# Optimization experiments

Hardware: AMD Instinct MI355X
Metric: run time of the kernel (lower is better)

The kernel has to match this reference:

```python
import jax, jax.numpy as jnp
import numpy as np

N_NODES = 100000
MAX_CHILD = 8
X_SIZE = 128
H_SIZE = 128
N_TYPES = 8
W_SCALE = 0.05  # keep gates out of saturation


def setup_inputs() -> dict:
    key = jax.random.key(0)
    ks = jax.random.split(key, 8)
    return {
        "x": jax.random.normal(ks[0], (N_NODES, X_SIZE), jnp.float32),
        "n_h": jax.random.normal(ks[1], (N_NODES, MAX_CHILD, H_SIZE), jnp.float32),
        "n_c": jax.random.normal(ks[2], (N_NODES, MAX_CHILD, H_SIZE), jnp.float32),
        "type_id": jax.random.randint(ks[3], (N_NODES,), 0, N_TYPES, jnp.int64),
        "W_iou": jax.random.normal(ks[4], (N_TYPES, X_SIZE, 3 * H_SIZE), jnp.float32) * W_SCALE,
        "U_iou": jax.random.normal(ks[5], (N_TYPES, H_SIZE, 3 * H_SIZE), jnp.float32) * W_SCALE,
        "b_iou": jnp.zeros((N_TYPES, 3 * H_SIZE), jnp.float32),
        "U_f": jax.random.normal(ks[6], (N_TYPES, H_SIZE, H_SIZE), jnp.float32) * W_SCALE,
        "b_f": jnp.zeros((N_TYPES, H_SIZE), jnp.float32),
    }


def reference(x, n_h, n_c, type_id, W_iou, U_iou, b_iou, U_f, b_f):
    # x: [N, X], n_h/n_c: [N, K, H] child mailbox, type_id: [N]
    N, K, H = n_h.shape
    T = W_iou.shape[0]
    h_sum = n_h.sum(axis=1)  # child-sum is linear -> aggregate before GEMM [N, H]

    # --- reduce_func: masked per-type child aggregation ---
    iou_aggr = jnp.zeros((N, 3 * H), x.dtype)
    c_aggr = jnp.zeros((N, H), x.dtype)
    for t in range(T):
        m = (type_id == t)[:, None]
        iou_t = h_sum @ U_iou[t]                                   # [N, 3H]
        f = jax.nn.sigmoid(jnp.einsum("nkh,hg->nkg", n_h, U_f[t]) + b_f[t])
        c_t = (f * n_c).sum(axis=1)                                # [N, H]
        iou_aggr = jnp.where(m, iou_t, iou_aggr)
        c_aggr = jnp.where(m, c_t, c_aggr)

    # --- apply_node_func: masked per-type node states ---
    h_out = jnp.zeros((N, H), x.dtype)
    c_out = jnp.zeros((N, H), x.dtype)
    for t in range(T):
        m = (type_id == t)[:, None]
        iou = x @ W_iou[t] + iou_aggr + b_iou[t]                   # [N, 3H]
        i_g, o_g, u_g = jnp.split(iou, 3, axis=1)
        c_t = jax.nn.sigmoid(i_g) * jnp.tanh(u_g) + c_aggr
        h_t = jax.nn.sigmoid(o_g) * jnp.tanh(c_t)
        h_out = jnp.where(m, h_t, h_out)
        c_out = jnp.where(m, c_t, c_out)
    return h_out, c_out
```

## Files before the change

kernel.cpp:

```cpp
#include <hip/hip_runtime.h>
#include <hip/hip_bf16.h>
#include <stdint.h>

typedef __bf16 bf16x8 __attribute__((ext_vector_type(8)));
typedef float  f32x4  __attribute__((ext_vector_type(4)));

#define H    128
#define KCH  8
#define NT   8
#define BM   32

#define WS_TILET  2048
#define WS_IDX    16384
#define WS_UF     458752
#define WS_W      720896

__device__ __forceinline__ float fsigm(float v){ return 1.f/(1.f+__expf(-v)); }
__device__ __forceinline__ float ftanh(float v){
  v = fminf(fmaxf(v,-15.f),15.f);
  float e = __expf(2.f*v);
  return (e-1.f)/(e+1.f);
}

__global__ void k_init(int* ws){ if (threadIdx.x < 40) ws[threadIdx.x] = 0; }

__global__ void k_detect(const int* __restrict__ type_id, int* ws){
  __shared__ int nz;
  if (threadIdx.x == 0) nz = 0;
  __syncthreads();
  int v = type_id[threadIdx.x];
  if ((threadIdx.x & 1) && v != 0) atomicAdd(&nz, 1);
  __syncthreads();
  if (threadIdx.x == 0) ws[25] = (nz == 0) ? 2 : 1;
}

__global__ void k_count(const int* __restrict__ type_id, int* __restrict__ ws, int N){
  __shared__ int h[NT];
  int tid = threadIdx.x;
  if (tid < NT) h[tid] = 0;
  __syncthreads();
  int stride = ws[25];
  int i = blockIdx.x*blockDim.x + tid;
  if (i < N) atomicAdd(&h[type_id[(size_t)i*stride]], 1);
  __syncthreads();
  if (tid < NT) atomicAdd(&ws[tid], h[tid]);
}

__global__ void k_scan(int* m){
  int s = 0;
  for (int t=0;t<NT;++t){
    m[16+t] = s;
    m[8+t]  = s;
    m[26+t] = s + m[t];
    s += ((m[t]+BM-1)/BM)*BM;
  }
  m[24] = s;
}

__global__ void k_scatter(const int* __restrict__ type_id, int* __restrict__ ws, int N){
  __shared__ int h[NT], base[NT];
  int tid = threadIdx.x;
  if (tid < NT) h[tid] = 0;
  __syncthreads();
  int stride = ws[25];
  int i = blockIdx.x*blockDim.x + tid;
  int t = 0, lp = 0;
  if (i < N){ t = type_id[(size_t)i*stride]; lp = atomicAdd(&h[t], 1); }
  __syncthreads();
  if (tid < NT) base[tid] = atomicAdd(&ws[8+tid], h[tid]);
  __syncthreads();
  if (i < N) ws[(WS_IDX/4) + base[t] + lp] = i;
}

__global__ void k_tiletype(int* ws, int ntiles){
  int i = blockIdx.x*256 + threadIdx.x;
  if (i >= ntiles) return;
  const int* op = ws + 16;
  int p = i*BM, t = -1;
  if (p < op[8]){
    for (int s=0;s<NT;++s) if (p >= op[s] && p < op[s+1]) t = s;
  }
  ws[(WS_TILET/4) + i] = t;
}

__global__ void k_prep_uf(const float* __restrict__ U_f, char* __restrict__ ws){
  int gid = blockIdx.x*256 + threadIdx.x;
  if (gid >= NT*128*16) return;
  int sp = gid & 15, c = (gid>>4) & 127, t = gid >> 11;
  int kbase = 8*(sp ^ (c & 7));
  const float* src = U_f + ((size_t)t*H + kbase)*H + c;
  bf16x8 v;
  #pragma unroll
  for (int j=0;j<8;++j) v[j] = (__bf16)src[(size_t)j*H];
  *(bf16x8*)(ws + WS_UF + (size_t)gid*16) = v;
}

__global__ void k_prep_w(const float* __restrict__ W_iou, const float* __restrict__ U_iou,
                         char* __restrict__ ws){
  int gid = blockIdx.x*256 + threadIdx.x;
  if (gid >= NT*384*32) return;
  int sp = gid & 31, col = (gid>>5) % 384, t = gid / (384*32);
  int K0 = sp*8;
  bf16x8 v;
  #pragma unroll
  for (int j=0;j<8;++j){
    int K = K0 + j;
    float f = (K < H) ? W_iou[((size_t)t*H + K)*(3*H) + col]
                      : U_iou[((size_t)t*H + (K-H))*(3*H) + col];
    v[j] = (__bf16)f;
  }
  *(bf16x8*)(ws + WS_W + (size_t)gid*16) = v;
}

__global__ __launch_bounds__(256,3) void k_fused(
  const float* __restrict__ x, const float* __restrict__ n_h, const float* __restrict__ n_c,
  const float* __restrict__ b_iou, const float* __restrict__ b_f,
  const char* __restrict__ ws, float* __restrict__ out, int N)
{
  __shared__ __align__(16) char lds[49152];
  const int* meta = (const int*)ws;
  int tile = blockIdx.x;
  int t = ((const int*)(ws + WS_TILET))[tile];
  if (t < 0) return;
  int ev = meta[26 + t];
  const int* idx = (const int*)(ws + WS_IDX);

  int tid = threadIdx.x;
  int lane = tid & 63, wave = tid >> 6;
  int rw = wave & 1, cw = wave >> 1;
  int l15 = lane & 15, l4 = lane >> 4;
  int base = tile*BM;

  int mrow = tid >> 3, mcol = (tid & 7) * 16;
  int mpos = base + mrow;
  int mnode = (mpos < ev) ? idx[mpos] : 0;

  int npos = base + rw*16 + l15;
  bool valn = npos < ev;
  int nd = valn ? idx[npos] : 0;
  const float* ncb = n_c + (size_t)nd*(KCH*H);
  int ocb[4]; f32x4 bf4[4];
  #pragma unroll
  for (int st=0; st<4; ++st){
    ocb[st] = cw*64 + st*16 + 4*l4;
    bf4[st] = *(const f32x4*)(b_f + t*H + ocb[st]);
  }

  {
    const char* src = ws + WS_UF + (size_t)t*32768;
    #pragma unroll
    for (int it=0; it<8; ++it){
      bf16x8 v = *(const bf16x8*)(src + it*4096 + tid*16);
      *(bf16x8*)(lds + it*4096 + tid*16) = v;
    }
  }

  const float* nh_base = n_h + (size_t)mnode*(KCH*H) + mcol;

  float hsum[16];
  #pragma unroll
  for (int j=0;j<16;++j) hsum[j] = 0.f;
  f32x4 cacc[4];
  #pragma unroll
  for (int st=0;st<4;++st) cacc[st] = (f32x4){0.f,0.f,0.f,0.f};

  int arow = rw*16 + l15;
  int aswz = (arow & 7) << 4;
  int mswz = (mrow & 7) << 4;

  {
    const float4* p = (const float4*)nh_base;
    float4 a0=p[0], a1=p[1], a2=p[2], a3=p[3];
    hsum[0]+=a0.x;  hsum[1]+=a0.y;  hsum[2]+=a0.z;  hsum[3]+=a0.w;
    hsum[4]+=a1.x;  hsum[5]+=a1.y;  hsum[6]+=a1.z;  hsum[7]+=a1.w;
    hsum[8]+=a2.x;  hsum[9]+=a2.y;  hsum[10]+=a2.z; hsum[11]+=a2.w;
    hsum[12]+=a3.x; hsum[13]+=a3.y; hsum[14]+=a3.z; hsum[15]+=a3.w;
    bf16x8 w0, w1;
    w0[0]=(__bf16)a0.x; w0[1]=(__bf16)a0.y; w0[2]=(__bf16)a0.z; w0[3]=(__bf16)a0.w;
    w0[4]=(__bf16)a1.x; w0[5]=(__bf16)a1.y; w0[6]=(__bf16)a1.z; w0[7]=(__bf16)a1.w;
    w1[0]=(__bf16)a2.x; w1[1]=(__bf16)a2.y; w1[2]=(__bf16)a2.z; w1[3]=(__bf16)a2.w;
    w1[4]=(__bf16)a3.x; w1[5]=(__bf16)a3.y; w1[6]=(__bf16)a3.z; w1[7]=(__bf16)a3.w;
    *(bf16x8*)(lds + 32768 + mrow*256 + (( mcol*2      ) ^ mswz)) = w0;
    *(bf16x8*)(lds + 32768 + mrow*256 + (( mcol*2 + 16 ) ^ mswz)) = w1;
  }
  __syncthreads();

  #pragma unroll 1
  for (int k=0;k<KCH;++k){
    const int cur = 32768 + (k&1)*8192;
    const int nxt = 32768 + ((k+1)&1)*8192;

    f32x4 nc4[4];
    #pragma unroll
    for (int st=0;st<4;++st) nc4[st] = *(const f32x4*)(ncb + (size_t)k*H + ocb[st]);

    float4 b0,b1,b2,b3;
    if (k < KCH-1){
      const float4* p = (const float4*)(nh_base + (size_t)(k+1)*H);
      b0=p[0]; b1=p[1]; b2=p[2]; b3=p[3];
    }

    f32x4 fa[4];
    #pragma unroll
    for (int st=0;st<4;++st) fa[st] = (f32x4){0.f,0.f,0.f,0.f};
    __builtin_amdgcn_s_setprio(1);
    #pragma unroll
    for (int kk=0; kk<4; ++kk){
      int kb = kk*64 + l4*16;
      bf16x8 bnh = *(const bf16x8*)(lds + cur + arow*256 + (kb ^ aswz));
      #pragma unroll
      for (int st=0;st<4;++st){
        int c = cw*64 + st*16 + l15;
        bf16x8 auf = *(const bf16x8*)(lds + c*256 + (kb ^ ((c&7)<<4)));
        fa[st] = __builtin_amdgcn_mfma_f32_16x16x32_bf16(auf, bnh, fa[st], 0,0,0);
      }
    }
    __builtin_amdgcn_s_setprio(0);

    if (k < KCH-1){
      hsum[0]+=b0.x;  hsum[1]+=b0.y;  hsum[2]+=b0.z;  hsum[3]+=b0.w;
      hsum[4]+=b1.x;  hsum[5]+=b1.y;  hsum[6]+=b1.z;  hsum[7]+=b1.w;
      hsum[8]+=b2.x;  hsum[9]+=b2.y;  hsum[10]+=b2.z; hsum[11]+=b2.w;
      hsum[12]+=b3.x; hsum[13]+=b3.y; hsum[14]+=b3.z; hsum[15]+=b3.w;
      bf16x8 w0, w1;
      w0[0]=(__bf16)b0.x; w0[1]=(__bf16)b0.y; w0[2]=(__bf16)b0.z; w0[3]=(__bf16)b0.w;
      w0[4]=(__bf16)b1.x; w0[5]=(__bf16)b1.y; w0[6]=(__bf16)b1.z; w0[7]=(__bf16)b1.w;
      w1[0]=(__bf16)b2.x; w1[1]=(__bf16)b2.y; w1[2]=(__bf16)b2.z; w1[3]=(__bf16)b2.w;
      w1[4]=(__bf16)b3.x; w1[5]=(__bf16)b3.y; w1[6]=(__bf16)b3.z; w1[7]=(__bf16)b3.w;
      *(bf16x8*)(lds + nxt + mrow*256 + (( mcol*2      ) ^ mswz)) = w0;
      *(bf16x8*)(lds + nxt + mrow*256 + (( mcol*2 + 16 ) ^ mswz)) = w1;
    }
    __syncthreads();

    #pragma unroll
    for (int st=0;st<4;++st){
      #pragma unroll
      for (int r=0;r<4;++r){
        float fg = fsigm(fa[st][r] + bf4[st][r]);
        cacc[st][r] += fg * nc4[st][r];
      }
    }
  }

  {
    const float4* px = (const float4*)(x + (size_t)mnode*H + mcol);
    float4 x0=px[0], x1=px[1], x2=px[2], x3=px[3];
    bf16x8 w0,w1,w2,w3;
    w0[0]=(__bf16)x0.x; w0[1]=(__bf16)x0.y; w0[2]=(__bf16)x0.z; w0[3]=(__bf16)x0.w;
    w0[4]=(__bf16)x1.x; w0[5]=(__bf16)x1.y; w0[6]=(__bf16)x1.z; w0[7]=(__bf16)x1.w;
    w1[0]=(__bf16)x2.x; w1[1]=(__bf16)x2.y; w1[2]=(__bf16)x2.z; w1[3]=(__bf16)x2.w;
    w1[4]=(__bf16)x3.x; w1[5]=(__bf16)x3.y; w1[6]=(__bf16)x3.z; w1[7]=(__bf16)x3.w;
    #pragma unroll
    for (int j=0;j<8;++j){ w2[j]=(__bf16)hsum[j]; w3[j]=(__bf16)hsum[8+j]; }
    int ab = 32768 + mrow*512;
    *(bf16x8*)(lds + ab + (( mcol*2            ) ^ mswz)) = w0;
    *(bf16x8*)(lds + ab + (( mcol*2 + 16       ) ^ mswz)) = w1;
    *(bf16x8*)(lds + ab + (( 256 + mcol*2      ) ^ mswz)) = w2;
    *(bf16x8*)(lds + ab + (( 256 + mcol*2 + 16 ) ^ mswz)) = w3;
  }
  __syncthreads();

  const char* wbase = ws + WS_W + (size_t)t*(384*256*2);
  #pragma unroll
  for (int st=0; st<4; ++st){
    f32x4 ag[3];
    #pragma unroll
    for (int g=0;g<3;++g) ag[g] = (f32x4){0.f,0.f,0.f,0.f};
    const char* wrow = wbase + (size_t)(cw*64 + st*16 + l15)*512;
    #pragma unroll 2
    for (int kc=0;kc<4;++kc){
      #pragma unroll
      for (int kk2=0;kk2<2;++kk2){
        int kb = kc*128 + kk2*64 + l4*16;
        bf16x8 bact = *(const bf16x8*)(lds + 32768 + arow*512 + (kb ^ aswz));
        #pragma unroll
        for (int g=0;g<3;++g){
          bf16x8 aW = *(const bf16x8*)(wrow + (size_t)(g*128)*512 + kb);
          ag[g] = __builtin_amdgcn_mfma_f32_16x16x32_bf16(aW, bact, ag[g], 0,0,0);
        }
      }
    }
    if (valn){
      f32x4 bi4 = *(const f32x4*)(b_iou + t*(3*H) +        ocb[st]);
      f32x4 bo4 = *(const f32x4*)(b_iou + t*(3*H) + H   +  ocb[st]);
      f32x4 bu4 = *(const f32x4*)(b_iou + t*(3*H) + 2*H +  ocb[st]);
      f32x4 hv4, cv4;
      #pragma unroll
      for (int r=0;r<4;++r){
        float ig = ag[0][r] + bi4[r];
        float og = ag[1][r] + bo4[r];
        float ug = ag[2][r] + bu4[r];
        float cv = fsigm(ig)*ftanh(ug) + cacc[st][r];
        float hv = fsigm(og)*ftanh(cv);
        cv4[r] = cv; hv4[r] = hv;
      }
      *(f32x4*)(out + (size_t)nd*H + ocb[st]) = hv4;
      *(f32x4*)(out + (size_t)N*H + (size_t)nd*H + ocb[st]) = cv4;
    }
  }
}

extern "C" void kernel_launch(void* const* d_in, const int* in_sizes, int n_in,
                              void* d_out, int out_size, void* d_ws, size_t ws_size,
                              hipStream_t stream){
  const float* x      = (const float*)d_in[0];
  const float* n_h    = (const float*)d_in[1];
  const float* n_c    = (const float*)d_in[2];
  const int*   typ    = (const int*)d_in[3];
  const float* W_iou  = (const float*)d_in[4];
  const float* U_iou  = (const float*)d_in[5];
  const float* b_iou  = (const float*)d_in[6];
  const float* U_f    = (const float*)d_in[7];
  const float* b_f    = (const float*)d_in[8];
  float* out = (float*)d_out;
  int*   ws  = (int*)d_ws;
  char*  wsc = (char*)d_ws;
  int N = in_sizes[0] / H;
  int nb = (N + 255) / 256;
  int ntiles = (N + NT*(BM-1) + BM-1) / BM;

  hipLaunchKernelGGL(k_init,     dim3(1),   dim3(64),  0, stream, ws);
  hipLaunchKernelGGL(k_detect,   dim3(1),   dim3(256), 0, stream, typ, ws);
  hipLaunchKernelGGL(k_count,    dim3(nb),  dim3(256), 0, stream, typ, ws, N);
  hipLaunchKernelGGL(k_scan,     dim3(1),   dim3(1),   0, stream, ws);
  hipLaunchKernelGGL(k_scatter,  dim3(nb),  dim3(256), 0, stream, typ, ws, N);
  hipLaunchKernelGGL(k_tiletype, dim3((ntiles+255)/256), dim3(256), 0, stream, ws, ntiles);
  hipLaunchKernelGGL(k_prep_uf,  dim3((NT*128*16+255)/256), dim3(256), 0, stream, U_f, wsc);
  hipLaunchKernelGGL(k_prep_w,   dim3((NT*384*32+255)/256), dim3(256), 0, stream, W_iou, U_iou, wsc);
  hipLaunchKernelGGL(k_fused,    dim3(ntiles), dim3(256), 0, stream,
                     x, n_h, n_c, b_iou, b_f, wsc, out, N);
}
```

Before: 347.7 us.

## Double fused kernel block to 512 threads, halving per-thread column work

Raises the fused TreeLSTM kernel from 256 to 512 threads per block. Each thread now handles 8 columns of the child-h staging instead of 16, and each wave covers 32 output columns instead of 64. The goal is more waves per tile to hide global-load latency and to cut register pressure, with launch bounds raised to ask for 4 blocks per CU. The cost is more barrier participants and the same LDS use per block, which may cap occupancy. The hidden tail (cw/rw mapping for 8 waves, the output write) must also agree with the new wave layout.

```diff
diff --git a/kernel.cpp b/kernel.cpp
--- a/kernel.cpp
+++ b/kernel.cpp
@@ -112,7 +112,7 @@
   *(bf16x8*)(ws + WS_W + (size_t)gid*16) = v;
 }
 
-__global__ __launch_bounds__(256,3) void k_fused(
+__global__ __launch_bounds__(512,4) void k_fused(
   const float* __restrict__ x, const float* __restrict__ n_h, const float* __restrict__ n_c,
   const float* __restrict__ b_iou, const float* __restrict__ b_f,
   const char* __restrict__ ws, float* __restrict__ out, int N)
@@ -131,7 +131,7 @@
   int l15 = lane & 15, l4 = lane >> 4;
   int base = tile*BM;
 
-  int mrow = tid >> 3, mcol = (tid & 7) * 16;
+  int mrow = tid >> 4, mcol8 = (tid & 15) * 8;
   int mpos = base + mrow;
   int mnode = (mpos < ev) ? idx[mpos] : 0;
 
@@ -139,30 +139,30 @@
   bool valn = npos < ev;
   int nd = valn ? idx[npos] : 0;
   const float* ncb = n_c + (size_t)nd*(KCH*H);
-  int ocb[4]; f32x4 bf4[4];
-  #pragma unroll
-  for (int st=0; st<4; ++st){
-    ocb[st] = cw*64 + st*16 + 4*l4;
+  int ocb[2]; f32x4 bf4[2];
+  #pragma unroll
+  for (int st=0; st<2; ++st){
+    ocb[st] = cw*32 + st*16 + 4*l4;
     bf4[st] = *(const f32x4*)(b_f + t*H + ocb[st]);
   }
 
   {
     const char* src = ws + WS_UF + (size_t)t*32768;
     #pragma unroll
-    for (int it=0; it<8; ++it){
-      bf16x8 v = *(const bf16x8*)(src + it*4096 + tid*16);
-      *(bf16x8*)(lds + it*4096 + tid*16) = v;
-    }
-  }
-
-  const float* nh_base = n_h + (size_t)mnode*(KCH*H) + mcol;
-
-  float hsum[16];
-  #pragma unroll
-  for (int j=0;j<16;++j) hsum[j] = 0.f;
-  f32x4 cacc[4];
-  #pragma unroll
-  for (int st=0;st<4;++st) cacc[st] = (f32x4){0.f,0.f,0.f,0.f};
+    for (int it=0; it<4; ++it){
+      bf16x8 v = *(const bf16x8*)(src + it*8192 + tid*16);
+      *(bf16x8*)(lds + it*8192 + tid*16) = v;
+    }
+  }
+
+  const float* nh_base = n_h + (size_t)mnode*(KCH*H) + mcol8;
+
+  float hsum[8];
+  #pragma unroll
+  for (int j=0;j<8;++j) hsum[j] = 0.f;
+  f32x4 cacc[2];
+  #pragma unroll
+  for (int st=0;st<2;++st) cacc[st] = (f32x4){0.f,0.f,0.f,0.f};
 
   int arow = rw*16 + l15;
   int aswz = (arow & 7) << 4;
@@ -170,18 +170,13 @@
 
   {
     const float4* p = (const float4*)nh_base;
-    float4 a0=p[0], a1=p[1], a2=p[2], a3=p[3];
-    hsum[0]+=a0.x;  hsum[1]+=a0.y;  hsum[2]+=a0.z;  hsum[3]+=a0.w;
-    hsum[4]+=a1.x;  hsum[5]+=a1.y;  hsum[6]+=a1.z;  hsum[7]+=a1.w;
-    hsum[8]+=a2.x;  hsum[9]+=a2.y;  hsum[10]+=a2.z; hsum[11]+=a2.w;
-    hsum[12]+=a3.x; hsum[13]+=a3.y; hsum[14]+=a3.z; hsum[15]+=a3.w;
-    bf16x8 w0, w1;
+    float4 a0=p[0], a1=p[1];
+    hsum[0]+=a0.x; hsum[1]+=a0.y; hsum[2]+=a0.z; hsum[3]+=a0.w;
+    hsum[4]+=a1.x; hsum[5]+=a1.y; hsum[6]+=a1.z; hsum[7]+=a1.w;
+    bf16x8 w0;
     w0[0]=(__bf16)a0.x; w0[1]=(__bf16)a0.y; w0[2]=(__bf16)a0.z; w0[3]=(__bf16)a0.w;
     w0[4]=(__bf16)a1.x; w0[5]=(__bf16)a1.y; w0[6]=(__bf16)a1.z; w0[7]=(__bf16)a1.w;
-    w1[0]=(__bf16)a2.x; w1[1]=(__bf16)a2.y; w1[2]=(__bf16)a2.z; w1[3]=(__bf16)a2.w;
-    w1[4]=(__bf16)a3.x; w1[5]=(__bf16)a3.y; w1[6]=(__bf16)a3.z; w1[7]=(__bf16)a3.w;
-    *(bf16x8*)(lds + 32768 + mrow*256 + (( mcol*2      ) ^ mswz)) = w0;
-    *(bf16x8*)(lds + 32768 + mrow*256 + (( mcol*2 + 16 ) ^ mswz)) = w1;
+    *(bf16x8*)(lds + 32768 + mrow*256 + (( mcol8*2 ) ^ mswz)) = w0;
   }
   __syncthreads();
 
@@ -190,27 +185,27 @@
     const int cur = 32768 + (k&1)*8192;
     const int nxt = 32768 + ((k+1)&1)*8192;
 
-    f32x4 nc4[4];
-    #pragma unroll
-    for (int st=0;st<4;++st) nc4[st] = *(const f32x4*)(ncb + (size_t)k*H + ocb[st]);
-
-    float4 b0,b1,b2,b3;
+    f32x4 nc4[2];
+    #pragma unroll
+    for (int st=0;st<2;++st) nc4[st] = *(const f32x4*)(ncb + (size_t)k*H + ocb[st]);
+
+    float4 b0,b1;
     if (k < KCH-1){
       const float4* p = (const float4*)(nh_base + (size_t)(k+1)*H);
-      b0=p[0]; b1=p[1]; b2=p[2]; b3=p[3];
-    }
-
-    f32x4 fa[4];
-    #pragma unroll
-    for (int st=0;st<4;++st) fa[st] = (f32x4){0.f,0.f,0.f,0.f};
+      b0=p[0]; b1=p[1];
+    }
+
+    f32x4 fa[2];
+    #pragma unroll
+    for (int st=0;st<2;++st) fa[st] = (f32x4){0.f,0.f,0.f,0.f};
     __builtin_amdgcn_s_setprio(1);
     #pragma unroll
     for (int kk=0; kk<4; ++kk){
       int kb = kk*64 + l4*16;
       bf16x8 bnh = *(const bf16x8*)(lds + cur + arow*256 + (kb ^ aswz));
       #pragma unroll
-      for (int st=0;st<4;++st){
-        int c = cw*64 + st*16 + l15;
+      for (int st=0;st<2;++st){
+        int c = cw*32 + st*16 + l15;
         bf16x8 auf = *(const bf16x8*)(lds + c*256 + (kb ^ ((c&7)<<4)));
         fa[st] = __builtin_amdgcn_mfma_f32_16x16x32_bf16(auf, bnh, fa[st], 0,0,0);
       }
@@ -218,22 +213,17 @@
     __builtin_amdgcn_s_setprio(0);
 
     if (k < KCH-1){
-      hsum[0]+=b0.x;  hsum[1]+=b0.y;  hsum[2]+=b0.z;  hsum[3]+=b0.w;
-      hsum[4]+=b1.x;  hsum[5]+=b1.y;  hsum[6]+=b1.z;  hsum[7]+=b1.w;
-      hsum[8]+=b2.x;  hsum[9]+=b2.y;  hsum[10]+=b2.z; hsum[11]+=b2.w;
-      hsum[12]+=b3.x; hsum[13]+=b3.y; hsum[14]+=b3.z; hsum[15]+=b3.w;
-      bf16x8 w0, w1;
+      hsum[0]+=b0.x; hsum[1]+=b0.y; hsum[2]+=b0.z; hsum[3]+=b0.w;
+      hsum[4]+=b1.x; hsum[5]+=b1.y; hsum[6]+=b1.z; hsum[7]+=b1.w;
+      bf16x8 w0;
       w0[0]=(__bf16)b0.x; w0[1]=(__bf16)b0.y; w0[2]=(__bf16)b0.z; w0[3]=(__bf16)b0.w;
       w0[4]=(__bf16)b1.x; w0[5]=(__bf16)b1.y; w0[6]=(__bf16)b1.z; w0[7]=(__bf16)b1.w;
-      w1[0]=(__bf16)b2.x; w1[1]=(__bf16)b2.y; w1[2]=(__bf16)b2.z; w1[3]=(__bf16)b2.w;
-      w1[4]=(__bf16)b3.x; w1[5]=(__bf16)b3.y; w1[6]=(__bf16)b3.z; w1[7]=(__bf16)b3.w;
-      *(bf16x8*)(lds + nxt + mrow*256 + (( mcol*2      ) ^ mswz)) = w0;
-      *(bf16x8*)(lds + nxt + mrow*256 + (( mcol*2 + 16 ) ^ mswz)) = w1;
+      *(bf16x8*)(lds + nxt + mrow*256 + (( mcol8*2 ) ^ mswz)) = w0;
     }
     __syncthreads();
 
     #pragma unroll
-    for (int st=0;st<4;++st){
+    for (int st=0;st<2;++st){
       #pragma unroll
       for (int r=0;r<4;++r){
         float fg = fsigm(fa[st][r] + bf4[st][r]);
@@ -243,30 +233,26 @@
   }
 
   {
-    const float4* px = (const float4*)(x + (size_t)mnode*H + mcol);
-    float4 x0=px[0], x1=px[1], x2=px[2], x3=px[3];
-    bf16x8 w0,w1,w2,w3;
+    const float4* px = (const float4*)(x + (size_t)mnode*H + mcol8);
+    float4 x0=px[0], x1=px[1];
+    bf16x8 w0, w2;
     w0[0]=(__bf16)x0.x; w0[1]=(__bf16)x0.y; w0[2]=(__bf16)x0.z; w0[3]=(__bf16)x0.w;
     w0[4]=(__bf16)x1.x; w0[5]=(__bf16)x1.y; w0[6]=(__bf16)x1.z; w0[7]=(__bf16)x1.w;
-    w1[0]=(__bf16)x2.x; w1[1]=(__bf16)x2.y; w1[2]=(__bf16)x2.z; w1[3]=(__bf16)x2.w;
-    w1[4]=(__bf16)x3.x; w1[5]=(__bf16)x3.y; w1[6]=(__bf16)x3.z; w1[7]=(__bf16)x3.w;
-    #pragma unroll
-    for (int j=0;j<8;++j){ w2[j]=(__bf16)hsum[j]; w3[j]=(__bf16)hsum[8+j]; }
+    #pragma unroll
+    for (int j=0;j<8;++j) w2[j]=(__bf16)hsum[j];
     int ab = 32768 + mrow*512;
-    *(bf16x8*)(lds + ab + (( mcol*2            ) ^ mswz)) = w0;
-    *(bf16x8*)(lds + ab + (( mcol*2 + 16       ) ^ mswz)) = w1;
-    *(bf16x8*)(lds + ab + (( 256 + mcol*2      ) ^ mswz)) = w2;
-    *(bf16x8*)(lds + ab + (( 256 + mcol*2 + 16 ) ^ mswz)) = w3;
+    *(bf16x8*)(lds + ab + (( mcol8*2       ) ^ mswz)) = w0;
+    *(bf16x8*)(lds + ab + (( 256 + mcol8*2 ) ^ mswz)) = w2;
   }
   __syncthreads();
 
   const char* wbase = ws + WS_W + (size_t)t*(384*256*2);
   #pragma unroll
-  for (int st=0; st<4; ++st){
+  for (int st=0; st<2; ++st){
     f32x4 ag[3];
     #pragma unroll
     for (int g=0;g<3;++g) ag[g] = (f32x4){0.f,0.f,0.f,0.f};
-    const char* wrow = wbase + (size_t)(cw*64 + st*16 + l15)*512;
+    const char* wrow = wbase + (size_t)(cw*32 + st*16 + l15)*512;
     #pragma unroll 2
     for (int kc=0;kc<4;++kc){
       #pragma unroll
@@ -327,6 +313,6 @@
   hipLaunchKernelGGL(k_tiletype, dim3((ntiles+255)/256), dim3(256), 0, stream, ws, ntiles);
   hipLaunchKernelGGL(k_prep_uf,  dim3((NT*128*16+255)/256), dim3(256), 0, stream, U_f, wsc);
   hipLaunchKernelGGL(k_prep_w,   dim3((NT*384*32+255)/256), dim3(256), 0, stream, W_iou, U_iou, wsc);
-  hipLaunchKernelGGL(k_fused,    dim3(ntiles), dim3(256), 0, stream,
+  hipLaunchKernelGGL(k_fused,    dim3(ntiles), dim3(512), 0, stream,
                      x, n_h, n_c, b_iou, b_f, wsc, out, N);
 }
```

New measurement: 373.5 us. +7.4%, slower.

## Split child loop across wave pairs and feed n_h directly as MFMA B operand

Applied to the files above, without the earlier changes.

Instead of staging each child's n_h row through LDS with double buffering and a barrier per child, each wave now loads n_h for its own 16 nodes straight from global memory into MFMA B-operand registers. The 8 children are split between the two wave halves (4 each), and the partial h-sum and c-aggregate are combined through LDS afterwards. This removes the 8 per-child syncthreads and the LDS round trip for n_h. In exchange it adds register pressure (16 f32x4 accumulators), a cross-wave reduction step, and less coalesced strided global loads of n_h and n_c.

```diff
diff --git a/kernel.cpp b/kernel.cpp
--- a/kernel.cpp
+++ b/kernel.cpp
@@ -127,24 +127,16 @@
 
   int tid = threadIdx.x;
   int lane = tid & 63, wave = tid >> 6;
-  int rw = wave & 1, cw = wave >> 1;
+  int rw = wave & 1, kh = wave >> 1;
   int l15 = lane & 15, l4 = lane >> 4;
   int base = tile*BM;
-
-  int mrow = tid >> 3, mcol = (tid & 7) * 16;
-  int mpos = base + mrow;
-  int mnode = (mpos < ev) ? idx[mpos] : 0;
 
   int npos = base + rw*16 + l15;
   bool valn = npos < ev;
   int nd = valn ? idx[npos] : 0;
+  const float* nhb = n_h + (size_t)nd*(KCH*H);
   const float* ncb = n_c + (size_t)nd*(KCH*H);
-  int ocb[4]; f32x4 bf4[4];
-  #pragma unroll
-  for (int st=0; st<4; ++st){
-    ocb[st] = cw*64 + st*16 + 4*l4;
-    bf4[st] = *(const f32x4*)(b_f + t*H + ocb[st]);
-  }
+  int node = rw*16 + l15;
 
   {
     const char* src = ws + WS_UF + (size_t)t*32768;
@@ -154,125 +146,121 @@
       *(bf16x8*)(lds + it*4096 + tid*16) = v;
     }
   }
-
-  const float* nh_base = n_h + (size_t)mnode*(KCH*H) + mcol;
-
-  float hsum[16];
+  __syncthreads();
+
+  f32x4 cacc[8], hsv[8];
   #pragma unroll
-  for (int j=0;j<16;++j) hsum[j] = 0.f;
-  f32x4 cacc[4];
-  #pragma unroll
-  for (int st=0;st<4;++st) cacc[st] = (f32x4){0.f,0.f,0.f,0.f};
-
-  int arow = rw*16 + l15;
-  int aswz = (arow & 7) << 4;
-  int mswz = (mrow & 7) << 4;
+  for (int i=0;i<8;++i){ cacc[i]=(f32x4){0,0,0,0}; hsv[i]=(f32x4){0,0,0,0}; }
+
+  #pragma unroll 1
+  for (int j=0;j<4;++j){
+    int k = kh*4 + j;
+    const float* rowp = nhb + (size_t)k*H + l4*8;
+    f32x4 L0 = *(const f32x4*)(rowp +  0);
+    f32x4 L1 = *(const f32x4*)(rowp +  4);
+    f32x4 L2 = *(const f32x4*)(rowp + 32);
+    f32x4 L3 = *(const f32x4*)(rowp + 36);
+    f32x4 L4 = *(const f32x4*)(rowp + 64);
+    f32x4 L5 = *(const f32x4*)(rowp + 68);
+    f32x4 L6 = *(const f32x4*)(rowp + 96);
+    f32x4 L7 = *(const f32x4*)(rowp +100);
+
+    hsv[0]+=L0; hsv[1]+=L1; hsv[2]+=L2; hsv[3]+=L3;
+    hsv[4]+=L4; hsv[5]+=L5; hsv[6]+=L6; hsv[7]+=L7;
+
+    bf16x8 bn0, bn1, bn2, bn3;
+    #pragma unroll
+    for (int jj=0;jj<4;++jj){
+      bn0[jj]=(__bf16)L0[jj]; bn0[4+jj]=(__bf16)L1[jj];
+      bn1[jj]=(__bf16)L2[jj]; bn1[4+jj]=(__bf16)L3[jj];
+      bn2[jj]=(__bf16)L4[jj]; bn2[4+jj]=(__bf16)L5[jj];
+      bn3[jj]=(__bf16)L6[jj]; bn3[4+jj]=(__bf16)L7[jj];
+    }
+
+    __builtin_amdgcn_s_setprio(1);
+    #pragma unroll
+    for (int st=0; st<8; ++st){
+      int c = st*16 + l15;
+      int cs = (c&7)<<4;
+      const char* crow = lds + c*256;
+      f32x4 fa = (f32x4){0,0,0,0};
+      fa = __builtin_amdgcn_mfma_f32_16x16x32_bf16(*(const bf16x8*)(crow + ((  0 + l4*16) ^ cs)), bn0, fa, 0,0,0);
+      fa = __builtin_amdgcn_mfma_f32_16x16x32_bf16(*(const bf16x8*)(crow + (( 64 + l4*16) ^ cs)), bn1, fa, 0,0,0);
+      fa = __builtin_amdgcn_mfma_f32_16x16x32_bf16(*(const bf16x8*)(crow + ((128 + l4*16) ^ cs)), bn2, fa, 0,0,0);
+      fa = __builtin_amdgcn_mfma_f32_16x16x32_bf16(*(const bf16x8*)(crow + ((192 + l4*16) ^ cs)), bn3, fa, 0,0,0);
+      f32x4 nc = *(const f32x4*)(ncb + (size_t)k*H + st*16 + 4*l4);
+      f32x4 bf = *(const f32x4*)(b_f + t*H + st*16 + 4*l4);
+      #pragma unroll
+      for (int r=0;r<4;++r)
+        cacc[st][r] += fsigm(fa[r] + bf[r]) * nc[r];
+    }
+    __builtin_amdgcn_s_setprio(0);
+  }
+
+  char* R = lds + 32768;
+  __syncthreads();
+  if (kh == 0){
+    #pragma unroll
+    for (int i=0;i<8;++i) *(f32x4*)(R + rw*8192 + i*1024 + lane*16) = hsv[i];
+  }
+  __syncthreads();
+  if (kh == 1){
+    #pragma unroll
+    for (int i=0;i<8;++i) hsv[i] += *(const f32x4*)(R + rw*8192 + i*1024 + lane*16);
+    #pragma unroll
+    for (int i=0;i<8;++i) *(f32x4*)(R + rw*8192 + i*1024 + lane*16) = cacc[i];
+  }
+  __syncthreads();
+  if (kh == 0){
+    #pragma unroll
+    for (int i=0;i<8;++i) cacc[i] += *(const f32x4*)(R + rw*8192 + i*1024 + lane*16);
+    #pragma unroll
+    for (int st=0;st<8;++st)
+      *(f32x4*)(lds + 16384 + node*512 + (((st*16 + 4*l4)*4) ^ ((l15&7)<<4))) = cacc[st];
+  } else {
+    #pragma unroll
+    for (int kk=0;kk<4;++kk){
+      bf16x8 w;
+      #pragma unroll
+      for (int jj=0;jj<4;++jj){ w[jj]=(__bf16)hsv[2*kk][jj]; w[4+jj]=(__bf16)hsv[2*kk+1][jj]; }
+      *(bf16x8*)(lds + node*512 + ((256 + (kk*32 + l4*8)*2) ^ ((node&7)<<4))) = w;
+    }
+  }
 
   {
-    const float4* p = (const float4*)nh_base;
-    float4 a0=p[0], a1=p[1], a2=p[2], a3=p[3];
-    hsum[0]+=a0.x;  hsum[1]+=a0.y;  hsum[2]+=a0.z;  hsum[3]+=a0.w;
-    hsum[4]+=a1.x;  hsum[5]+=a1.y;  hsum[6]+=a1.z;  hsum[7]+=a1.w;
-    hsum[8]+=a2.x;  hsum[9]+=a2.y;  hsum[10]+=a2.z; hsum[11]+=a2.w;
-    hsum[12]+=a3.x; hsum[13]+=a3.y; hsum[14]+=a3.z; hsum[15]+=a3.w;
-    bf16x8 w0, w1;
-    w0[0]=(__bf16)a0.x; w0[1]=(__bf16)a0.y; w0[2]=(__bf16)a0.z; w0[3]=(__bf16)a0.w;
-    w0[4]=(__bf16)a1.x; w0[5]=(__bf16)a1.y; w0[6]=(__bf16)a1.z; w0[7]=(__bf16)a1.w;
-    w1[0]=(__bf16)a2.x; w1[1]=(__bf16)a2.y; w1[2]=(__bf16)a2.z; w1[3]=(__bf16)a2.w;
-    w1[4]=(__bf16)a3.x; w1[5]=(__bf16)a3.y; w1[6]=(__bf16)a3.z; w1[7]=(__bf16)a3.w;
-    *(bf16x8*)(lds + 32768 + mrow*256 + (( mcol*2      ) ^ mswz)) = w0;
-    *(bf16x8*)(lds + 32768 + mrow*256 + (( mcol*2 + 16 ) ^ mswz)) = w1;
-  }
-  __syncthreads();
-
-  #pragma unroll 1
-  for (int k=0;k<KCH;++k){
-    const int cur = 32768 + (k&1)*8192;
-    const int nxt = 32768 + ((k+1)&1)*8192;
-
-    f32x4 nc4[4];
-    #pragma unroll
-    for (int st=0;st<4;++st) nc4[st] = *(const f32x4*)(ncb + (size_t)k*H + ocb[st]);
-
-    float4 b0,b1,b2,b3;
-    if (k < KCH-1){
-      const float4* p = (const float4*)(nh_base + (size_t)(k+1)*H);
-      b0=p[0]; b1=p[1]; b2=p[2]; b3=p[3];
-    }
-
-    f32x4 fa[4];
-    #pragma unroll
-    for (int st=0;st<4;++st) fa[st] = (f32x4){0.f,0.f,0.f,0.f};
-    __builtin_amdgcn_s_setprio(1);
-    #pragma unroll
-    for (int kk=0; kk<4; ++kk){
-      int kb = kk*64 + l4*16;
-      bf16x8 bnh = *(const bf16x8*)(lds + cur + arow*256 + (kb ^ aswz));
-      #pragma unroll
-      for (int st=0;st<4;++st){
-        int c = cw*64 + st*16 + l15;
-        bf16x8 auf = *(const bf16x8*)(lds + c*256 + (kb ^ ((c&7)<<4)));
-        fa[st] = __builtin_amdgcn_mfma_f32_16x16x32_bf16(auf, bnh, fa[st], 0,0,0);
-      }
-    }
-    __builtin_amdgcn_s_setprio(0);
-
-    if (k < KCH-1){
-      hsum[0]+=b0.x;  hsum[1]+=b0.y;  hsum[2]+=b0.z;  hsum[3]+=b0.w;
-      hsum[4]+=b1.x;  hsum[5]+=b1.y;  hsum[6]+=b1.z;  hsum[7]+=b1.w;
-      hsum[8]+=b2.x;  hsum[9]+=b2.y;  hsum[10]+=b2.z; hsum[11]+=b2.w;
-      hsum[12]+=b3.x; hsum[13]+=b3.y; hsum[14]+=b3.z; hsum[15]+=b3.w;
-      bf16x8 w0, w1;
-      w0[0]=(__bf16)b0.x; w0[1]=(__bf16)b0.y; w0[2]=(__bf16)b0.z; w0[3]=(__bf16)b0.w;
-      w0[4]=(__bf16)b1.x; w0[5]=(__bf16)b1.y; w0[6]=(__bf16)b1.z; w0[7]=(__bf16)b1.w;
-      w1[0]=(__bf16)b2.x; w1[1]=(__bf16)b2.y; w1[2]=(__bf16)b2.z; w1[3]=(__bf16)b2.w;
-      w1[4]=(__bf16)b3.x; w1[5]=(__bf16)b3.y; w1[6]=(__bf16)b3.z; w1[7]=(__bf16)b3.w;
-      *(bf16x8*)(lds + nxt + mrow*256 + (( mcol*2      ) ^ mswz)) = w0;
-      *(bf16x8*)(lds + nxt + mrow*256 + (( mcol*2 + 16 ) ^ mswz)) = w1;
-    }
-    __syncthreads();
-
-    #pragma unroll
-    for (int st=0;st<4;++st){
-      #pragma unroll
-      for (int r=0;r<4;++r){
-        float fg = fsigm(fa[st][r] + bf4[st][r]);
-        cacc[st][r] += fg * nc4[st][r];
-      }
-    }
-  }
-
-  {
+    int mrow = tid >> 3, mcol = (tid & 7) * 16;
+    int mpos = base + mrow;
+    int mnode = (mpos < ev) ? idx[mpos] : 0;
+    int mswz = (mrow & 7) << 4;
     const float4* px = (const float4*)(x + (size_t)mnode*H + mcol);
     float4 x0=px[0], x1=px[1], x2=px[2], x3=px[3];
-    bf16x8 w0,w1,w2,w3;
+    bf16x8 w0,w1;
     w0[0]=(__bf16)x0.x; w0[1]=(__bf16)x0.y; w0[2]=(__bf16)x0.z; w0[3]=(__bf16)x0.w;
     w0[4]=(__bf16)x1.x; w0[5]=(__bf16)x1.y; w0[6]=(__bf16)x1.z; w0[7]=(__bf16)x1.w;
     w1[0]=(__bf16)x2.x; w1[1]=(__bf16)x2.y; w1[2]=(__bf16)x2.z; w1[3]=(__bf16)x2.w;
     w1[4]=(__bf16)x3.x; w1[5]=(__bf16)x3.y; w1[6]=(__bf16)x3.z; w1[7]=(__bf16)x3.w;
-    #pragma unroll
-    for (int j=0;j<8;++j){ w2[j]=(__bf16)hsum[j]; w3[j]=(__bf16)hsum[8+j]; }
-    int ab = 32768 + mrow*512;
-    *(bf16x8*)(lds + ab + (( mcol*2            ) ^ mswz)) = w0;
-    *(bf16x8*)(lds + ab + (( mcol*2 + 16       ) ^ mswz)) = w1;
-    *(bf16x8*)(lds + ab + (( 256 + mcol*2      ) ^ mswz)) = w2;
-    *(bf16x8*)(lds + ab + (( 256 + mcol*2 + 16 ) ^ mswz)) = w3;
-  }
-  __syncthreads();
-
+    *(bf16x8*)(lds + mrow*512 + (( mcol*2      ) ^ mswz)) = w0;
+    *(bf16x8*)(lds + mrow*512 + (( mcol*2 + 16 ) ^ mswz)) = w1;
+  }
+  __syncthreads();
+
+  int cw = kh;
+  int arow = node;
+  int aswz = (arow & 7) << 4;
   const char* wbase = ws + WS_W + (size_t)t*(384*256*2);
   #pragma unroll
   for (int st=0; st<4; ++st){
+    int ocb = cw*64 + st*16 + 4*l4;
     f32x4 ag[3];
     #pragma unroll
-    for (int g=0;g<3;++g) ag[g] = (f32x4){0.f,0.f,0.f,0.f};
+    for (int g=0;g<3;++g) ag[g] = (f32x4){0,0,0,0};
     const char* wrow = wbase + (size_t)(cw*64 + st*16 + l15)*512;
     #pragma unroll 2
     for (int kc=0;kc<4;++kc){
       #pragma unroll
       for (int kk2=0;kk2<2;++kk2){
         int kb = kc*128 + kk2*64 + l4*16;
-        bf16x8 bact = *(const bf16x8*)(lds + 32768 + arow*512 + (kb ^ aswz));
+        bf16x8 bact = *(const bf16x8*)(lds + arow*512 + (kb ^ aswz));
         #pragma unroll
         for (int g=0;g<3;++g){
           bf16x8 aW = *(const bf16x8*)(wrow + (size_t)(g*128)*512 + kb);
@@ -281,21 +269,22 @@
       }
     }
     if (valn){
-      f32x4 bi4 = *(const f32x4*)(b_iou + t*(3*H) +        ocb[st]);
-      f32x4 bo4 = *(const f32x4*)(b_iou + t*(3*H) + H   +  ocb[st]);
-      f32x4 bu4 = *(const f32x4*)(b_iou + t*(3*H) + 2*H +  ocb[st]);
+      f32x4 bi4 = *(const f32x4*)(b_iou + t*(3*H) +        ocb);
+      f32x4 bo4 = *(const f32x4*)(b_iou + t*(3*H) + H   +  ocb);
+      f32x4 bu4 = *(const f32x4*)(b_iou + t*(3*H) + 2*H +  ocb);
+      f32x4 ca  = *(const f32x4*)(lds + 16384 + node*512 + ((ocb*4) ^ ((l15&7)<<4)));
       f32x4 hv4, cv4;
       #pragma unroll
       for (int r=0;r<4;++r){
         float ig = ag[0][r] + bi4[r];
         float og = ag[1][r] + bo4[r];
         float ug = ag[2][r] + bu4[r];
-        float cv = fsigm(ig)*ftanh(ug) + cacc[st][r];
+        float cv = fsigm(ig)*ftanh(ug) + ca[r];
         float hv = fsigm(og)*ftanh(cv);
         cv4[r] = cv; hv4[r] = hv;
       }
-      *(f32x4*)(out + (size_t)nd*H + ocb[st]) = hv4;
-      *(f32x4*)(out + (size_t)N*H + (size_t)nd*H + ocb[st]) = cv4;
+      *(f32x4*)(out + (size_t)nd*H + ocb) = hv4;
+      *(f32x4*)(out + (size_t)N*H + (size_t)nd*H + ocb) = cv4;
     }
   }
 }
```

After: 605.1 us. 1.74x slower.
